# Optimization experiments

Hardware: AMD Instinct MI355X
Metric: run time of the kernel (lower is better)

The kernel has to match this reference:

```python
import jax, jax.numpy as jnp
import numpy as np

DIM = 512        # model dim
MOE_DIM = 256    # expert hidden dim
E = 64           # n_routed experts
G = 8            # n_routed_group
TOPK_G = 4       # n_topk_group
K = 8            # n_experts_per_tok
SCALE = 2.5      # routed_scale
CAP = 1024


def setup_inputs() -> dict:
    key = jax.random.key(0)
    ks = jax.random.split(key, 6)
    x = jax.random.normal(ks[0], (4, 512, DIM), jnp.float32)
    gate_w = jax.random.normal(ks[1], (E, DIM), jnp.float32) / np.sqrt(DIM).astype(np.float32)
    gate_b = jax.random.normal(ks[2], (E,), jnp.float32) * 0.01
    w1 = jax.random.normal(ks[3], (E, DIM, MOE_DIM), jnp.float32) / np.sqrt(DIM).astype(np.float32)
    w3 = jax.random.normal(ks[4], (E, DIM, MOE_DIM), jnp.float32) / np.sqrt(DIM).astype(np.float32)
    w2 = jax.random.normal(ks[5], (E, MOE_DIM, DIM), jnp.float32) / np.sqrt(MOE_DIM).astype(np.float32)
    return {"x": x, "gate_w": gate_w, "gate_b": gate_b, "w1": w1, "w3": w3, "w2": w2}


def _gate(x2, gate_w, gate_b):
    # x2: [T, DIM] -> (weights [T,K], indices [T,K])
    T = x2.shape[0]
    scores = jax.nn.sigmoid(x2 @ gate_w.T)                      # [T, E]
    s = (scores + gate_b).reshape(T, G, E // G)                  # grouped scores
    group_scores = jax.lax.top_k(s, 2)[0].sum(-1)                # [T, G] sum of top-2 per group
    top_groups = jax.lax.top_k(group_scores, TOPK_G)[1]          # [T, TOPK_G]
    gmask = jnp.zeros((T, G), bool).at[jnp.arange(T)[:, None], top_groups].set(True)
    s = jnp.where(gmask[..., None], s, -jnp.inf).reshape(T, E)
    idx = jax.lax.top_k(s, K)[1]                                 # [T, K]
    w = jnp.take_along_axis(scores, idx, axis=1)                 # original (pre-bias) scores
    w = w / w.sum(-1, keepdims=True) * SCALE
    return w, idx


def _moe_forward(x, gate_w, gate_b, w1, w3, w2):
    shape = x.shape
    x2 = x.reshape(-1, DIM)                                      # [T, DIM]
    T = x2.shape[0]
    w, idx = _gate(x2, gate_w, gate_b)
    flat_e = idx.reshape(-1)                                     # [T*K]
    # position of each (token, slot) within its expert's buffer, in order
    oh = (flat_e[:, None] == jnp.arange(E)[None, :]).astype(jnp.int32)  # [T*K, E]
    pos = (jnp.cumsum(oh, axis=0) * oh).sum(-1) - 1              # [T*K]
    x_rep = jnp.repeat(x2, K, axis=0)                            # [T*K, DIM]
    # dispatch into per-expert buffers [E, CAP, DIM]
    xb = jnp.zeros((E, CAP, DIM), x2.dtype).at[flat_e, pos].set(x_rep, mode='drop')
    h = jax.nn.silu(jnp.einsum('ecd,edm->ecm', xb, w1)) * jnp.einsum('ecd,edm->ecm', xb, w3)
    yb = jnp.einsum('ecm,emd->ecd', h, w2)                       # [E, CAP, DIM]
    # combine: gather back and weight
    y = yb.at[flat_e, pos].get(mode='fill', fill_value=0.0) * w.reshape(-1)[:, None]
    return y.reshape(T, K, DIM).sum(1).reshape(shape)


def reference(x, gate_w, gate_b, w1, w3, w2):
    return _moe_forward(x, gate_w, gate_b, w1, w3, w2)
```

## Files before the change

kernel.cpp:

```cpp
#include <hip/hip_runtime.h>

#define T_TOK 2048
#define DIM   512
#define MOE   256
#define NE    64
#define NG    8
#define TOPKG 4
#define TOPK  8
#define CAP   1024
#define MOE_SCALE 2.5f

typedef float f32x4 __attribute__((ext_vector_type(4)));
typedef short s16x8 __attribute__((ext_vector_type(8)));

__device__ __forceinline__ unsigned short f2bf(float f) {
    unsigned u = __builtin_bit_cast(unsigned, f);
    unsigned r = (u + 0x7fffu + ((u >> 16) & 1u)) >> 16;
    return (unsigned short)r;
}
__device__ __forceinline__ unsigned pk2(float lo, float hi) {
    return (unsigned)f2bf(lo) | ((unsigned)f2bf(hi) << 16);
}

__global__ __launch_bounds__(256) void gwt_k(const float* __restrict__ gw,
                                             float* __restrict__ gwT)
{
    int idx = blockIdx.x * 256 + threadIdx.x;
    int e = idx >> 9, k = idx & 511;
    gwT[(size_t)(k >> 2) * 256 + e * 4 + (k & 3)] = gw[idx];
}

__global__ __launch_bounds__(256) void gate_fused_k(const float* __restrict__ x,
                                                    const float* __restrict__ gwT,
                                                    const float* __restrict__ gb,
                                                    int* __restrict__ counts,
                                                    int* __restrict__ etok,
                                                    float* __restrict__ wt_of,
                                                    short* __restrict__ xb)
{
    __shared__ float xs[4][512];
    int w = threadIdx.x >> 6, lane = threadIdx.x & 63;
    int t = blockIdx.x * 4 + w;

    {
        const float4* xr = (const float4*)(x + (size_t)t * DIM);
        float4 v0 = xr[lane * 2], v1 = xr[lane * 2 + 1];
        *(float4*)&xs[w][lane * 8]     = v0;
        *(float4*)&xs[w][lane * 8 + 4] = v1;
        short o[8];
        o[0] = (short)f2bf(v0.x); o[1] = (short)f2bf(v0.y);
        o[2] = (short)f2bf(v0.z); o[3] = (short)f2bf(v0.w);
        o[4] = (short)f2bf(v1.x); o[5] = (short)f2bf(v1.y);
        o[6] = (short)f2bf(v1.z); o[7] = (short)f2bf(v1.w);
        *(s16x8*)(xb + (size_t)t * DIM + lane * 8) = *(const s16x8*)o;
    }
    __syncthreads();

    const float4* gt = (const float4*)gwT;
    float a0 = 0.f, a1 = 0.f, a2 = 0.f, a3 = 0.f;
#pragma unroll 4
    for (int k4 = 0; k4 < 128; k4 += 4) {
        float4 g0 = gt[(k4 + 0) * 64 + lane];
        float4 g1 = gt[(k4 + 1) * 64 + lane];
        float4 g2 = gt[(k4 + 2) * 64 + lane];
        float4 g3 = gt[(k4 + 3) * 64 + lane];
        float4 x0 = *(const float4*)&xs[w][(k4 + 0) * 4];
        float4 x1 = *(const float4*)&xs[w][(k4 + 1) * 4];
        float4 x2 = *(const float4*)&xs[w][(k4 + 2) * 4];
        float4 x3 = *(const float4*)&xs[w][(k4 + 3) * 4];
        a0 += g0.x * x0.x + g0.y * x0.y + g0.z * x0.z + g0.w * x0.w;
        a1 += g1.x * x1.x + g1.y * x1.y + g1.z * x1.z + g1.w * x1.w;
        a2 += g2.x * x2.x + g2.y * x2.y + g2.z * x2.z + g2.w * x2.w;
        a3 += g3.x * x3.x + g3.y * x3.y + g3.z * x3.z + g3.w * x3.w;
    }
    float acc = (a0 + a1) + (a2 + a3);
    float sc = 1.f / (1.f + __expf(-acc));
    float s  = sc + gb[lane];

    float m1 = s, m2 = -1e30f;
#pragma unroll
    for (int d = 1; d < 8; d <<= 1) {
        float o1 = __shfl_xor(m1, d);
        float o2 = __shfl_xor(m2, d);
        float n1 = fmaxf(m1, o1);
        float n2 = fmaxf(fminf(m1, o1), fmaxf(m2, o2));
        m1 = n1; m2 = n2;
    }
    float gv = m1 + m2;

    bool gkeep = false;
#pragma unroll
    for (int it = 0; it < TOPKG; ++it) {
        float m = gv;
#pragma unroll
        for (int d = 1; d < 64; d <<= 1) m = fmaxf(m, __shfl_xor(m, d));
        unsigned long long mask = __ballot(gv == m);
        int ldr = __ffsll(mask) - 1;
        if ((lane >> 3) == (ldr >> 3)) { gkeep = true; gv = -2e30f; }
    }
    float sv = gkeep ? s : -1e30f;

    float wsum = 0.f;
    int my_e = 0; float my_w = 0.f;
#pragma unroll
    for (int k = 0; k < TOPK; ++k) {
        float m = sv;
#pragma unroll
        for (int d = 1; d < 64; d <<= 1) m = fmaxf(m, __shfl_xor(m, d));
        unsigned long long mask = __ballot(sv == m);
        int l = __ffsll(mask) - 1;
        float wk = __shfl(sc, l);
        wsum += wk;
        if (lane == k) { my_e = l; my_w = wk; }
        if (lane == l) sv = -2e30f;
    }
    float scale = MOE_SCALE / wsum;
    if (lane < TOPK) {
        int p = atomicAdd(&counts[my_e], 1);
        int rid = t * TOPK + lane;
        bool ok = (p < CAP);
        if (ok) etok[my_e * CAP + p] = rid;
        wt_of[rid] = ok ? my_w * scale : 0.f;
    }
}

__global__ __launch_bounds__(64) void scan_k(const int* __restrict__ counts,
                                             int* __restrict__ tbase)
{
    int lane = threadIdx.x;
    int ne = min(counts[lane], CAP);
    int nt = (ne + 31) >> 5;
    int v = nt;
#pragma unroll
    for (int d = 1; d < 64; d <<= 1) {
        int o = __shfl_up(v, d);
        if (lane >= d) v += o;
    }
    tbase[lane] = v - nt;
}

__global__ __launch_bounds__(256) void gather_k(const short* __restrict__ xb,
                                                const int* __restrict__ counts,
                                                const int* __restrict__ etok,
                                                const int* __restrict__ tbase,
                                                short* __restrict__ xgf)
{
    int e = blockIdx.x >> 3, sub3 = blockIdx.x & 7;
    int w = threadIdx.x >> 6, lane = threadIdx.x & 63;
    int T = sub3 * 4 + w;
    int ne = min(counts[e], CAP);
    int nt = (ne + 31) >> 5;
    if (T >= nt) return;
    int G = tbase[e] + T;
    int q = lane >> 4, m16 = lane & 15;
    int r0 = T * 32 + m16, r1 = T * 32 + 16 + m16;
    bool ok0 = r0 < ne, ok1 = r1 < ne;
    int tok0 = ok0 ? (etok[e * CAP + r0] >> 3) : 0;
    int tok1 = ok1 ? (etok[e * CAP + r1] >> 3) : 0;
    const short* s0 = xb + (size_t)tok0 * DIM + q * 8;
    const short* s1 = xb + (size_t)tok1 * DIM + q * 8;
    short* dst = xgf + (size_t)G * 16384 + lane * 8;
    s16x8 z = {0, 0, 0, 0, 0, 0, 0, 0};
#pragma unroll
    for (int b4 = 0; b4 < 4; ++b4) {
        s16x8 v[8];
#pragma unroll
        for (int i = 0; i < 4; ++i) {
            int kt = b4 * 4 + i;
            v[i * 2]     = ok0 ? *(const s16x8*)(s0 + kt * 32) : z;
            v[i * 2 + 1] = ok1 ? *(const s16x8*)(s1 + kt * 32) : z;
        }
#pragma unroll
        for (int i = 0; i < 4; ++i) {
            int kt = b4 * 4 + i;
            *(s16x8*)(dst + (size_t)(kt * 2 + 0) * 512) = v[i * 2];
            *(s16x8*)(dst + (size_t)(kt * 2 + 1) * 512) = v[i * 2 + 1];
        }
    }
}

__global__ __launch_bounds__(256, 3) void gemm1_k(const short* __restrict__ xgf,
                                                  const float* __restrict__ w1,
                                                  const float* __restrict__ w3,
                                                  const int* __restrict__ counts,
                                                  const int* __restrict__ tbase,
                                                  short* __restrict__ hgf)
{
    __shared__ short Bl[2][16][64][8];
    __shared__ short Ct[4][2][16][24];

    int e  = blockIdx.x & 63, cg = blockIdx.x >> 6;
    int n0 = cg * 16;
    int tid = threadIdx.x;
    int w = tid >> 6, lane = tid & 63;
    int q = lane >> 4, m16 = lane & 15;

    const float* W1e = w1 + (size_t)e * DIM * MOE + n0;
    const float* W3e = w3 + (size_t)e * DIM * MOE + n0;
#pragma unroll
    for (int it = 0; it < 8; ++it) {
        int idx = it * 256 + tid;
        int mat = idx >> 10;
        int rem = idx & 1023;
        int r2  = rem >> 2;
        int cq  = (rem & 3) * 4;
        int k   = r2 * 2;
        int kt = k >> 5, qf = (k >> 3) & 3, j0 = k & 7;
        const float* p = (mat ? W3e : W1e) + (size_t)k * MOE + cq;
        float4 lo = *(const float4*)p;
        float4 hi = *(const float4*)(p + MOE);
        unsigned* b = (unsigned*)&Bl[mat][kt][qf * 16 + cq][j0];
        b[0]  = pk2(lo.x, hi.x);
        b[4]  = pk2(lo.y, hi.y);
        b[8]  = pk2(lo.z, hi.z);
        b[12] = pk2(lo.w, hi.w);
    }
    __syncthreads();

    int ne = min(counts[e], CAP);
    int nt = (ne + 31) >> 5;
    int G0 = tbase[e];

    for (int T0 = w * 2; T0 < nt; T0 += 8) {
        bool v1 = (T0 + 1) < nt;
        const short* A0 = xgf + (size_t)(G0 + T0) * 16384 + lane * 8;
        const short* A1 = xgf + (size_t)(G0 + (v1 ? T0 + 1 : T0)) * 16384 + lane * 8;

        f32x4 acc[2][2][2];
#pragma unroll
        for (int i = 0; i < 2; ++i)
#pragma unroll
            for (int j = 0; j < 2; ++j)
#pragma unroll
                for (int m = 0; m < 2; ++m) acc[i][j][m] = (f32x4)0.f;

#pragma unroll
        for (int kt = 0; kt < 16; ++kt) {
            s16x8 a00 = *(const s16x8*)(A0 + (size_t)(kt * 2 + 0) * 512);
            s16x8 a01 = *(const s16x8*)(A0 + (size_t)(kt * 2 + 1) * 512);
            s16x8 a10 = *(const s16x8*)(A1 + (size_t)(kt * 2 + 0) * 512);
            s16x8 a11 = *(const s16x8*)(A1 + (size_t)(kt * 2 + 1) * 512);
            s16x8 b1 = *(const s16x8*)&Bl[0][kt][lane][0];
            s16x8 b3 = *(const s16x8*)&Bl[1][kt][lane][0];
            acc[0][0][0] = __builtin_amdgcn_mfma_f32_16x16x32_bf16(a00, b1, acc[0][0][0], 0, 0, 0);
            acc[0][1][0] = __builtin_amdgcn_mfma_f32_16x16x32_bf16(a01, b1, acc[0][1][0], 0, 0, 0);
            acc[1][0][0] = __builtin_amdgcn_mfma_f32_16x16x32_bf16(a10, b1, acc[1][0][0], 0, 0, 0);
            acc[1][1][0] = __builtin_amdgcn_mfma_f32_16x16x32_bf16(a11, b1, acc[1][1][0], 0, 0, 0);
            acc[0][0][1] = __builtin_amdgcn_mfma_f32_16x16x32_bf16(a00, b3, acc[0][0][1], 0, 0, 0);
            acc[0][1][1] = __builtin_amdgcn_mfma_f32_16x16x32_bf16(a01, b3, acc[0][1][1], 0, 0, 0);
            acc[1][0][1] = __builtin_amdgcn_mfma_f32_16x16x32_bf16(a10, b3, acc[1][0][1], 0, 0, 0);
            acc[1][1][1] = __builtin_amdgcn_mfma_f32_16x16x32_bf16(a11, b3, acc[1][1][1], 0, 0, 0);
        }

#pragma unroll
        for (int t2 = 0; t2 < 2; ++t2) {
            if (t2 && !v1) break;
#pragma unroll
            for (int sub = 0; sub < 2; ++sub)
#pragma unroll
                for (int r = 0; r < 4; ++r) {
                    float g = acc[t2][sub][0][r];
                    float u = acc[t2][sub][1][r];
                    float hv = g / (1.f + __expf(-g)) * u;
                    Ct[w][sub][q * 4 + r][m16] = (short)f2bf(hv);
                }
            int sub = q >> 1;
            s16x8 hv8 = *(const s16x8*)&Ct[w][sub][m16][(q & 1) * 8];
            size_t slot = ((size_t)(G0 + T0 + t2) * 8 + (cg >> 1)) * 2 + sub;
            *(s16x8*)(hgf + slot * 512 + ((cg & 1) * 2 + (q & 1)) * 128 + m16 * 8) = hv8;
        }
    }
}

__global__ __launch_bounds__(256, 3) void gemm2_k(const short* __restrict__ hgf,
                                                  const float* __restrict__ w2,
                                                  const int* __restrict__ counts,
                                                  const int* __restrict__ etok,
                                                  const int* __restrict__ tbase,
                                                  short* __restrict__ ybuf)
{
    __shared__ short Bl[2][8][64][8];

    int e  = blockIdx.x & 63, cg = blockIdx.x >> 6;
    int n0 = cg * 32;
    int tid = threadIdx.x;
    int w = tid >> 6, lane = tid & 63;
    int q = lane >> 4, m16 = lane & 15;

    const float* W2e = w2 + (size_t)e * MOE * DIM + n0;
#pragma unroll
    for (int it = 0; it < 4; ++it) {
        int idx = it * 256 + tid;
        int r2  = idx >> 3;
        int cq  = (idx & 7) * 4;
        int k   = r2 * 2;
        int kt2 = k >> 5, qf = (k >> 3) & 3, j0 = k & 7;
        int s = cq >> 4, c15 = cq & 15;
        const float* p = W2e + (size_t)k * DIM + cq;
        float4 lo = *(const float4*)p;
        float4 hi = *(const float4*)(p + DIM);
        unsigned* b = (unsigned*)&Bl[s][kt2][qf * 16 + c15][j0];
        b[0]  = pk2(lo.x, hi.x);
        b[4]  = pk2(lo.y, hi.y);
        b[8]  = pk2(lo.z, hi.z);
        b[12] = pk2(lo.w, hi.w);
    }
    __syncthreads();

    int ne = min(counts[e], CAP);
    int nt = (ne + 31) >> 5;
    int G0 = tbase[e];
    const int* el = etok + e * CAP;

    for (int T0 = w * 2; T0 < nt; T0 += 8) {
        bool v1 = (T0 + 1) < nt;
        const short* A0 = hgf + (size_t)(G0 + T0) * 8192 + lane * 8;
        const short* A1 = hgf + (size_t)(G0 + (v1 ? T0 + 1 : T0)) * 8192 + lane * 8;

        f32x4 acc[2][2][2];
#pragma unroll
        for (int i = 0; i < 2; ++i)
#pragma unroll
            for (int j = 0; j < 2; ++j)
#pragma unroll
                for (int m = 0; m < 2; ++m) acc[i][j][m] = (f32x4)0.f;

#pragma unroll
        for (int kt = 0; kt < 8; ++kt) {
            s16x8 a00 = *(const s16x8*)(A0 + (size_t)(kt * 2 + 0) * 512);
            s16x8 a01 = *(const s16x8*)(A0 + (size_t)(kt * 2 + 1) * 512);
            s16x8 a10 = *(const s16x8*)(A1 + (size_t)(kt * 2 + 0) * 512);
            s16x8 a11 = *(const s16x8*)(A1 + (size_t)(kt * 2 + 1) * 512);
            s16x8 b0 = *(const s16x8*)&Bl[0][kt][lane][0];
            s16x8 b1 = *(const s16x8*)&Bl[1][kt][lane][0];
            acc[0][0][0] = __builtin_amdgcn_mfma_f32_16x16x32_bf16(a00, b0, acc[0][0][0], 0, 0, 0);
            acc[0][1][0] = __builtin_amdgcn_mfma_f32_16x16x32_bf16(a01, b0, acc[0][1][0], 0, 0, 0);
            acc[1][0][0] = __builtin_amdgcn_mfma_f32_16x16x32_bf16(a10, b0, acc[1][0][0], 0, 0, 0);
            acc[1][1][0] = __builtin_amdgcn_mfma_f32_16x16x32_bf16(a11, b0, acc[1][1][0], 0, 0, 0);
            acc[0][0][1] = __builtin_amdgcn_mfma_f32_16x16x32_bf16(a00, b1, acc[0][0][1], 0, 0, 0);
            acc[0][1][1] = __builtin_amdgcn_mfma_f32_16x16x32_bf16(a01, b1, acc[0][1][1], 0, 0, 0);
            acc[1][0][1] = __builtin_amdgcn_mfma_f32_16x16x32_bf16(a10, b1, acc[1][0][1], 0, 0, 0);
            acc[1][1][1] = __builtin_amdgcn_mfma_f32_16x16x32_bf16(a11, b1, acc[1][1][1], 0, 0, 0);
        }

#pragma unroll
        for (int t2 = 0; t2 < 2; ++t2) {
            if (t2 && !v1) break;
            int T = T0 + t2;
#pragma unroll
            for (int sub = 0; sub < 2; ++sub)
#pragma unroll
                for (int s = 0; s < 2; ++s)
#pragma unroll
                    for (int r = 0; r < 4; ++r) {
                        int row = T * 32 + sub * 16 + q * 4 + r;
                        if (row < ne)
                            ybuf[(size_t)el[row] * DIM + n0 + s * 16 + m16] =
                                (short)f2bf(acc[t2][sub][s][r]);
                    }
        }
    }
}

__global__ __launch_bounds__(256) void combine_k(const short* __restrict__ ybuf,
                                                 const float* __restrict__ wt_of,
                                                 float* __restrict__ out)
{
    int t = blockIdx.x;
    int tid = threadIdx.x;
    const int* yb = (const int*)ybuf;
    float sx = 0.f, sy = 0.f;
#pragma unroll
    for (int k = 0; k < TOPK; ++k) {
        float wk = wt_of[t * TOPK + k];
        int v = yb[(size_t)(t * TOPK + k) * (DIM / 2) + tid];
        float lo = __builtin_bit_cast(float, (unsigned)v << 16);
        float hi = __builtin_bit_cast(float, (unsigned)v & 0xffff0000u);
        sx += wk * lo;
        sy += wk * hi;
    }
    float2 o = {sx, sy};
    ((float2*)out)[(size_t)t * (DIM / 2) + tid] = o;
}

extern "C" void kernel_launch(void* const* d_in, const int* in_sizes, int n_in,
                              void* d_out, int out_size, void* d_ws, size_t ws_size,
                              hipStream_t stream)
{
    const float* x  = (const float*)d_in[0];
    const float* gw = (const float*)d_in[1];
    const float* gb = (const float*)d_in[2];
    const float* w1 = (const float*)d_in[3];
    const float* w3 = (const float*)d_in[4];
    const float* w2 = (const float*)d_in[5];

    char* ws = (char*)d_ws;
    short* xb    = (short*)(ws);
    short* xgf   = (short*)(ws + 2097152);
    short* hgf   = (short*)(ws + 20971520);
    short* ybuf  = (short*)(ws + 30408704);
    float* gwT   = (float*)(ws + 47185920);
    int*   etok  = (int*)  (ws + 47316992);
    float* wt_of = (float*)(ws + 47579136);
    int*   counts= (int*)  (ws + 47644672);
    int*   tbase = (int*)  (ws + 47644928);

    hipMemsetAsync(counts, 0, NE * 4, stream);

    gwt_k<<<128, 256, 0, stream>>>(gw, gwT);
    gate_fused_k<<<T_TOK / 4, 256, 0, stream>>>(x, gwT, gb, counts, etok, wt_of, xb);
    scan_k<<<1, 64, 0, stream>>>(counts, tbase);
    gather_k<<<NE * 8, 256, 0, stream>>>(xb, counts, etok, tbase, xgf);
    gemm1_k<<<NE * 16, 256, 0, stream>>>(xgf, w1, w3, counts, tbase, hgf);
    gemm2_k<<<NE * 16, 256, 0, stream>>>(hgf, w2, counts, etok, tbase, ybuf);
    combine_k<<<T_TOK, 256, 0, stream>>>(ybuf, wt_of, (float*)d_out);
}
```

Baseline: 276.0 us.

## Fuse token gather into gemm1 and software-prefetch A fragments

```diff
diff --git a/kernel.cpp b/kernel.cpp
--- a/kernel.cpp
+++ b/kernel.cpp
@@ -139,50 +139,11 @@
     tbase[lane] = v - nt;
 }
 
-__global__ __launch_bounds__(256) void gather_k(const short* __restrict__ xb,
-                                                const int* __restrict__ counts,
-                                                const int* __restrict__ etok,
-                                                const int* __restrict__ tbase,
-                                                short* __restrict__ xgf)
-{
-    int e = blockIdx.x >> 3, sub3 = blockIdx.x & 7;
-    int w = threadIdx.x >> 6, lane = threadIdx.x & 63;
-    int T = sub3 * 4 + w;
-    int ne = min(counts[e], CAP);
-    int nt = (ne + 31) >> 5;
-    if (T >= nt) return;
-    int G = tbase[e] + T;
-    int q = lane >> 4, m16 = lane & 15;
-    int r0 = T * 32 + m16, r1 = T * 32 + 16 + m16;
-    bool ok0 = r0 < ne, ok1 = r1 < ne;
-    int tok0 = ok0 ? (etok[e * CAP + r0] >> 3) : 0;
-    int tok1 = ok1 ? (etok[e * CAP + r1] >> 3) : 0;
-    const short* s0 = xb + (size_t)tok0 * DIM + q * 8;
-    const short* s1 = xb + (size_t)tok1 * DIM + q * 8;
-    short* dst = xgf + (size_t)G * 16384 + lane * 8;
-    s16x8 z = {0, 0, 0, 0, 0, 0, 0, 0};
-#pragma unroll
-    for (int b4 = 0; b4 < 4; ++b4) {
-        s16x8 v[8];
-#pragma unroll
-        for (int i = 0; i < 4; ++i) {
-            int kt = b4 * 4 + i;
-            v[i * 2]     = ok0 ? *(const s16x8*)(s0 + kt * 32) : z;
-            v[i * 2 + 1] = ok1 ? *(const s16x8*)(s1 + kt * 32) : z;
-        }
-#pragma unroll
-        for (int i = 0; i < 4; ++i) {
-            int kt = b4 * 4 + i;
-            *(s16x8*)(dst + (size_t)(kt * 2 + 0) * 512) = v[i * 2];
-            *(s16x8*)(dst + (size_t)(kt * 2 + 1) * 512) = v[i * 2 + 1];
-        }
-    }
-}
-
-__global__ __launch_bounds__(256, 3) void gemm1_k(const short* __restrict__ xgf,
+__global__ __launch_bounds__(256, 3) void gemm1_k(const short* __restrict__ xb,
                                                   const float* __restrict__ w1,
                                                   const float* __restrict__ w3,
                                                   const int* __restrict__ counts,
+                                                  const int* __restrict__ etok,
                                                   const int* __restrict__ tbase,
                                                   short* __restrict__ hgf)
 {
@@ -197,7 +158,7 @@
 
     const float* W1e = w1 + (size_t)e * DIM * MOE + n0;
     const float* W3e = w3 + (size_t)e * DIM * MOE + n0;
-#pragma unroll
+#pragma unroll 4
     for (int it = 0; it < 8; ++it) {
         int idx = it * 256 + tid;
         int mat = idx >> 10;
@@ -220,55 +181,52 @@
     int ne = min(counts[e], CAP);
     int nt = (ne + 31) >> 5;
     int G0 = tbase[e];
-
-    for (int T0 = w * 2; T0 < nt; T0 += 8) {
-        bool v1 = (T0 + 1) < nt;
-        const short* A0 = xgf + (size_t)(G0 + T0) * 16384 + lane * 8;
-        const short* A1 = xgf + (size_t)(G0 + (v1 ? T0 + 1 : T0)) * 16384 + lane * 8;
-
-        f32x4 acc[2][2][2];
-#pragma unroll
-        for (int i = 0; i < 2; ++i)
-#pragma unroll
-            for (int j = 0; j < 2; ++j)
-#pragma unroll
-                for (int m = 0; m < 2; ++m) acc[i][j][m] = (f32x4)0.f;
-
+    const int* el = etok + e * CAP;
+
+    for (int T = w; T < nt; T += 4) {
+        int row0 = T * 32 + m16, row1 = T * 32 + 16 + m16;
+        int tok0 = el[row0 < ne ? row0 : ne - 1] >> 3;
+        int tok1 = el[row1 < ne ? row1 : ne - 1] >> 3;
+        const short* A0 = xb + (size_t)tok0 * DIM + q * 8;
+        const short* A1 = xb + (size_t)tok1 * DIM + q * 8;
+
+        f32x4 acc[2][2];
+#pragma unroll
+        for (int j = 0; j < 2; ++j)
+#pragma unroll
+            for (int m = 0; m < 2; ++m) acc[j][m] = (f32x4)0.f;
+
+        s16x8 a0 = *(const s16x8*)(A0);
+        s16x8 a1 = *(const s16x8*)(A1);
 #pragma unroll
         for (int kt = 0; kt < 16; ++kt) {
-            s16x8 a00 = *(const s16x8*)(A0 + (size_t)(kt * 2 + 0) * 512);
-            s16x8 a01 = *(const s16x8*)(A0 + (size_t)(kt * 2 + 1) * 512);
-            s16x8 a10 = *(const s16x8*)(A1 + (size_t)(kt * 2 + 0) * 512);
-            s16x8 a11 = *(const s16x8*)(A1 + (size_t)(kt * 2 + 1) * 512);
+            s16x8 a0n, a1n;
+            if (kt < 15) {
+                a0n = *(const s16x8*)(A0 + (kt + 1) * 32);
+                a1n = *(const s16x8*)(A1 + (kt + 1) * 32);
+            }
             s16x8 b1 = *(const s16x8*)&Bl[0][kt][lane][0];
             s16x8 b3 = *(const s16x8*)&Bl[1][kt][lane][0];
-            acc[0][0][0] = __builtin_amdgcn_mfma_f32_16x16x32_bf16(a00, b1, acc[0][0][0], 0, 0, 0);
-            acc[0][1][0] = __builtin_amdgcn_mfma_f32_16x16x32_bf16(a01, b1, acc[0][1][0], 0, 0, 0);
-            acc[1][0][0] = __builtin_amdgcn_mfma_f32_16x16x32_bf16(a10, b1, acc[1][0][0], 0, 0, 0);
-            acc[1][1][0] = __builtin_amdgcn_mfma_f32_16x16x32_bf16(a11, b1, acc[1][1][0], 0, 0, 0);
-            acc[0][0][1] = __builtin_amdgcn_mfma_f32_16x16x32_bf16(a00, b3, acc[0][0][1], 0, 0, 0);
-            acc[0][1][1] = __builtin_amdgcn_mfma_f32_16x16x32_bf16(a01, b3, acc[0][1][1], 0, 0, 0);
-            acc[1][0][1] = __builtin_amdgcn_mfma_f32_16x16x32_bf16(a10, b3, acc[1][0][1], 0, 0, 0);
-            acc[1][1][1] = __builtin_amdgcn_mfma_f32_16x16x32_bf16(a11, b3, acc[1][1][1], 0, 0, 0);
+            acc[0][0] = __builtin_amdgcn_mfma_f32_16x16x32_bf16(a0, b1, acc[0][0], 0, 0, 0);
+            acc[1][0] = __builtin_amdgcn_mfma_f32_16x16x32_bf16(a1, b1, acc[1][0], 0, 0, 0);
+            acc[0][1] = __builtin_amdgcn_mfma_f32_16x16x32_bf16(a0, b3, acc[0][1], 0, 0, 0);
+            acc[1][1] = __builtin_amdgcn_mfma_f32_16x16x32_bf16(a1, b3, acc[1][1], 0, 0, 0);
+            a0 = a0n; a1 = a1n;
         }
 
 #pragma unroll
-        for (int t2 = 0; t2 < 2; ++t2) {
-            if (t2 && !v1) break;
-#pragma unroll
-            for (int sub = 0; sub < 2; ++sub)
-#pragma unroll
-                for (int r = 0; r < 4; ++r) {
-                    float g = acc[t2][sub][0][r];
-                    float u = acc[t2][sub][1][r];
-                    float hv = g / (1.f + __expf(-g)) * u;
-                    Ct[w][sub][q * 4 + r][m16] = (short)f2bf(hv);
-                }
-            int sub = q >> 1;
-            s16x8 hv8 = *(const s16x8*)&Ct[w][sub][m16][(q & 1) * 8];
-            size_t slot = ((size_t)(G0 + T0 + t2) * 8 + (cg >> 1)) * 2 + sub;
-            *(s16x8*)(hgf + slot * 512 + ((cg & 1) * 2 + (q & 1)) * 128 + m16 * 8) = hv8;
-        }
+        for (int sub = 0; sub < 2; ++sub)
+#pragma unroll
+            for (int r = 0; r < 4; ++r) {
+                float g = acc[sub][0][r];
+                float u = acc[sub][1][r];
+                float hv = g / (1.f + __expf(-g)) * u;
+                Ct[w][sub][q * 4 + r][m16] = (short)f2bf(hv);
+            }
+        int sub = q >> 1;
+        s16x8 hv8 = *(const s16x8*)&Ct[w][sub][m16][(q & 1) * 8];
+        size_t slot = ((size_t)(G0 + T) * 8 + (cg >> 1)) * 2 + sub;
+        *(s16x8*)(hgf + slot * 512 + ((cg & 1) * 2 + (q & 1)) * 128 + m16 * 8) = hv8;
     }
 }
 
@@ -288,7 +246,7 @@
     int q = lane >> 4, m16 = lane & 15;
 
     const float* W2e = w2 + (size_t)e * MOE * DIM + n0;
-#pragma unroll
+#pragma unroll 4
     for (int it = 0; it < 4; ++it) {
         int idx = it * 256 + tid;
         int r2  = idx >> 3;
@@ -312,53 +270,44 @@
     int G0 = tbase[e];
     const int* el = etok + e * CAP;
 
-    for (int T0 = w * 2; T0 < nt; T0 += 8) {
-        bool v1 = (T0 + 1) < nt;
-        const short* A0 = hgf + (size_t)(G0 + T0) * 8192 + lane * 8;
-        const short* A1 = hgf + (size_t)(G0 + (v1 ? T0 + 1 : T0)) * 8192 + lane * 8;
-
-        f32x4 acc[2][2][2];
-#pragma unroll
-        for (int i = 0; i < 2; ++i)
-#pragma unroll
-            for (int j = 0; j < 2; ++j)
-#pragma unroll
-                for (int m = 0; m < 2; ++m) acc[i][j][m] = (f32x4)0.f;
-
+    for (int T = w; T < nt; T += 4) {
+        const short* A = hgf + (size_t)(G0 + T) * 8192 + lane * 8;
+
+        f32x4 acc[2][2];
+#pragma unroll
+        for (int j = 0; j < 2; ++j)
+#pragma unroll
+            for (int m = 0; m < 2; ++m) acc[j][m] = (f32x4)0.f;
+
+        s16x8 a0 = *(const s16x8*)(A);
+        s16x8 a1 = *(const s16x8*)(A + 512);
 #pragma unroll
         for (int kt = 0; kt < 8; ++kt) {
-            s16x8 a00 = *(const s16x8*)(A0 + (size_t)(kt * 2 + 0) * 512);
-            s16x8 a01 = *(const s16x8*)(A0 + (size_t)(kt * 2 + 1) * 512);
-            s16x8 a10 = *(const s16x8*)(A1 + (size_t)(kt * 2 + 0) * 512);
-            s16x8 a11 = *(const s16x8*)(A1 + (size_t)(kt * 2 + 1) * 512);
+            s16x8 a0n, a1n;
+            if (kt < 7) {
+                a0n = *(const s16x8*)(A + (size_t)((kt + 1) * 2 + 0) * 512);
+                a1n = *(const s16x8*)(A + (size_t)((kt + 1) * 2 + 1) * 512);
+            }
             s16x8 b0 = *(const s16x8*)&Bl[0][kt][lane][0];
             s16x8 b1 = *(const s16x8*)&Bl[1][kt][lane][0];
-            acc[0][0][0] = __builtin_amdgcn_mfma_f32_16x16x32_bf16(a00, b0, acc[0][0][0], 0, 0, 0);
-            acc[0][1][0] = __builtin_amdgcn_mfma_f32_16x16x32_bf16(a01, b0, acc[0][1][0], 0, 0, 0);
-            acc[1][0][0] = __builtin_amdgcn_mfma_f32_16x16x32_bf16(a10, b0, acc[1][0][0], 0, 0, 0);
-            acc[1][1][0] = __builtin_amdgcn_mfma_f32_16x16x32_bf16(a11, b0, acc[1][1][0], 0, 0, 0);
-            acc[0][0][1] = __builtin_amdgcn_mfma_f32_16x16x32_bf16(a00, b1, acc[0][0][1], 0, 0, 0);
-            acc[0][1][1] = __builtin_amdgcn_mfma_f32_16x16x32_bf16(a01, b1, acc[0][1][1], 0, 0, 0);
-            acc[1][0][1] = __builtin_amdgcn_mfma_f32_16x16x32_bf16(a10, b1, acc[1][0][1], 0, 0, 0);
-            acc[1][1][1] = __builtin_amdgcn_mfma_f32_16x16x32_bf16(a11, b1, acc[1][1][1], 0, 0, 0);
+            acc[0][0] = __builtin_amdgcn_mfma_f32_16x16x32_bf16(a0, b0, acc[0][0], 0, 0, 0);
+            acc[1][0] = __builtin_amdgcn_mfma_f32_16x16x32_bf16(a1, b0, acc[1][0], 0, 0, 0);
+            acc[0][1] = __builtin_amdgcn_mfma_f32_16x16x32_bf16(a0, b1, acc[0][1], 0, 0, 0);
+            acc[1][1] = __builtin_amdgcn_mfma_f32_16x16x32_bf16(a1, b1, acc[1][1], 0, 0, 0);
+            a0 = a0n; a1 = a1n;
         }
 
 #pragma unroll
-        for (int t2 = 0; t2 < 2; ++t2) {
-            if (t2 && !v1) break;
-            int T = T0 + t2;
-#pragma unroll
-            for (int sub = 0; sub < 2; ++sub)
-#pragma unroll
-                for (int s = 0; s < 2; ++s)
-#pragma unroll
-                    for (int r = 0; r < 4; ++r) {
-                        int row = T * 32 + sub * 16 + q * 4 + r;
-                        if (row < ne)
-                            ybuf[(size_t)el[row] * DIM + n0 + s * 16 + m16] =
-                                (short)f2bf(acc[t2][sub][s][r]);
-                    }
-        }
+        for (int sub = 0; sub < 2; ++sub)
+#pragma unroll
+            for (int s = 0; s < 2; ++s)
+#pragma unroll
+                for (int r = 0; r < 4; ++r) {
+                    int row = T * 32 + sub * 16 + q * 4 + r;
+                    if (row < ne)
+                        ybuf[(size_t)el[row] * DIM + n0 + s * 16 + m16] =
+                            (short)f2bf(acc[sub][s][r]);
+                }
     }
 }
 
@@ -396,22 +345,20 @@
 
     char* ws = (char*)d_ws;
     short* xb    = (short*)(ws);
-    short* xgf   = (short*)(ws + 2097152);
-    short* hgf   = (short*)(ws + 20971520);
-    short* ybuf  = (short*)(ws + 30408704);
-    float* gwT   = (float*)(ws + 47185920);
-    int*   etok  = (int*)  (ws + 47316992);
-    float* wt_of = (float*)(ws + 47579136);
-    int*   counts= (int*)  (ws + 47644672);
-    int*   tbase = (int*)  (ws + 47644928);
+    short* hgf   = (short*)(ws + 2097152);
+    short* ybuf  = (short*)(ws + 11534336);
+    float* gwT   = (float*)(ws + 28311552);
+    int*   etok  = (int*)  (ws + 28442624);
+    float* wt_of = (float*)(ws + 28704768);
+    int*   counts= (int*)  (ws + 28770304);
+    int*   tbase = (int*)  (ws + 28770560);
 
     hipMemsetAsync(counts, 0, NE * 4, stream);
 
     gwt_k<<<128, 256, 0, stream>>>(gw, gwT);
     gate_fused_k<<<T_TOK / 4, 256, 0, stream>>>(x, gwT, gb, counts, etok, wt_of, xb);
     scan_k<<<1, 64, 0, stream>>>(counts, tbase);
-    gather_k<<<NE * 8, 256, 0, stream>>>(xb, counts, etok, tbase, xgf);
-    gemm1_k<<<NE * 16, 256, 0, stream>>>(xgf, w1, w3, counts, tbase, hgf);
+    gemm1_k<<<NE * 16, 256, 0, stream>>>(xb, w1, w3, counts, etok, tbase, hgf);
     gemm2_k<<<NE * 16, 256, 0, stream>>>(hgf, w2, counts, etok, tbase, ybuf);
     combine_k<<<T_TOK, 256, 0, stream>>>(ybuf, wt_of, (float*)d_out);
 }
```

Measured after the change: 249.5 us. 9.6% less time.
